# Kernel tuning notes

Measured on AMD Instinct MI355X. Metric: run time of the kernel, lower is better.

## Reference

```python
import jax, jax.numpy as jnp
import numpy as np

B, K, N = 8192, 10, 100
LAM = 1.0


def _vec_transpose_P():
    # 9x9 vec-transpose permutation: P[3i+j, 3j+i] = 1 (the _getP matrix)
    P = np.zeros((9, 9), dtype=np.float32)
    for i in range(3):
        for j in range(3):
            P[3 * i + j, 3 * j + i] = 1.0
    return jnp.asarray(P)


def setup_inputs() -> dict:
    key = jax.random.key(0)
    k1, k2, k3 = jax.random.split(key, 3)
    weights = jax.random.uniform(k1, (N, 1), dtype=jnp.float32) + 0.1  # positive weights
    model_keypoints = jax.random.normal(k2, (K, 3, N), dtype=jnp.float32)
    y = jax.random.normal(k3, (B, 3, N), dtype=jnp.float32)
    return {"y": y, "weights": weights, "model_keypoints": model_keypoints}


def _pace_forward(y, weights, model_keypoints):
    n = model_keypoints.shape[-1]
    k = model_keypoints.shape[0]
    bsz = y.shape[0]
    w = weights                                  # (N,1)
    wsum = w.sum()
    b = model_keypoints                          # (K,3,N)
    b_w = (b @ w) / wsum                         # (K,3,1)
    sw = jnp.sqrt(w[:, 0])                       # (N,)

    # ---- precomputed constants (original __init__) ----
    bar_b = sw[None, None, :] * (b - b_w)                    # (K,3,N)
    bar_B = bar_b.transpose(0, 2, 1).reshape(k, 3 * n).T     # (3N,K), row idx 3n+a
    bar_H = 2.0 * (bar_B.T @ bar_B + LAM * jnp.eye(k, dtype=y.dtype))
    Hinv = jnp.linalg.inv(bar_H)
    Ht = Hinv @ jnp.ones((k, 1), dtype=y.dtype)
    denom = Ht.sum()
    G = Hinv - (Ht @ Ht.T) / denom               # (K,K)
    g = Ht / denom                               # (K,1)
    GBt = G @ bar_B.T                            # (K,3N)
    M = jnp.concatenate([2.0 * bar_B @ GBt - jnp.eye(3 * n, dtype=y.dtype),
                         2.0 * jnp.sqrt(LAM) * GBt], axis=0)       # (3N+K,3N)
    h = jnp.concatenate([bar_B @ g, jnp.sqrt(LAM) * g], axis=0)    # (3N+K,1)
    P = _vec_transpose_P().astype(y.dtype)

    # ---- forward ----
    y_w = (y @ w) / wsum                         # (B,3,1)
    bar_y = sw[None, None, :] * (y - y_w)        # (B,3,N)

    # E_b = M @ kron(Ybar_b^T, I3) @ P, done batched without materializing kron:
    # (M @ kron(Y^T, I3))[m, 3j+a] = sum_n M[m, 3n+a] * Y[j, n]
    Mr = M.reshape(-1, n, 3)                                  # Mr[m, nn, a] = M[m, 3nn+a]
    MB = jnp.einsum('mna,bjn->bmja', Mr, bar_y)               # (B,3N+K,3,3)
    E = MB.reshape(bsz, -1, 9) @ P                            # (B,3N+K,9)
    q00 = h[:, 0] @ h[:, 0]                                   # scalar h^T h
    hE = jnp.einsum('m,bmc->bc', h[:, 0], E)                  # (B,9)
    Q11 = jnp.einsum('bmc,bmd->bcd', E, E)                    # (B,9,9)
    top = jnp.concatenate([jnp.broadcast_to(q00, (bsz, 1, 1)), hE[:, None, :]], axis=2)
    bot = jnp.concatenate([hE[:, :, None], Q11], axis=2)
    Q = jnp.concatenate([top, bot], axis=1)                   # (B,10,10)

    # SDP relaxation: at a tight optimum X = v v^T with v the minimizer of v^T Q v,
    # recovered here as the eigenvector of Q with smallest eigenvalue (batched eigh)
    _, evec = jnp.linalg.eigh(Q)
    v = evec[:, :, 0]                                         # (B,10), ascending order
    v = v / v[:, :1]                                          # homogenize: v[0] = 1
    R = v[:, 1:].reshape(bsz, 3, 3).transpose(0, 2, 1)        # (B,3,3)

    # shape coefficients: c = 2 * G B^T * kron(I_N, R^T) vec(bar_y) + g
    RTy = jnp.einsum('bra,brn->bna', R, bar_y).reshape(bsz, 3 * n)   # idx 3n+a
    c = 2.0 * jnp.einsum('km,bm->bk', GBt, RTy)[:, :, None] + g[None, :, :]  # (B,K,1)
    # translation: t = y_w - R b_w^T c
    t = y_w - R @ jnp.einsum('ka,bko->bao', b_w[:, :, 0], c)  # (B,3,1)
    return R, t, c


def reference(y, weights, model_keypoints):
    return _pace_forward(y, weights, model_keypoints)
```

## Files before the change

kernel.cpp:

```cpp
#include <hip/hip_runtime.h>
#include <math.h>

#define SM_WSUM 0
#define SM_RWS  1
#define SM_Q00  2
#define SM_Z2   4
#define SM_BS   16
#define SM_W    48
#define SM_G    148
#define SM_GV   248
#define SM_BW   260
#define SM_SIZE 292

#define AR_W    0
#define AR_BW   104
#define AR_C    136
#define AR_HI   240
#define AR_G    340
#define AR_T    440
#define AR_GV   544
#define AR_HT   560
#define AR_Z    576
#define AR_F    0
#define AR_QL   360
#define AR_D    592
#define AR_G3   640
#define AR_SIZE 768

__host__ __device__ constexpr int TRI(int p,int q){ return p*10-(p*(p+1))/2+q; }
__host__ __device__ constexpr int SIDX(int a,int b){ return (a<=b)?TRI(a,b):TRI(b,a); }
__host__ __device__ constexpr int LTRI(int i,int j){ return i*(i+1)/2+j; }

template<int CTRL>
__device__ __forceinline__ float dpp_add(float v){
  int s = __builtin_amdgcn_mov_dpp(__float_as_int(v), CTRL, 0xF, 0xF, true);
  return v + __int_as_float(s);
}
__device__ __forceinline__ float gsum16(float v){
  v = dpp_add<0xB1>(v);
  v = dpp_add<0x4E>(v);
  v = dpp_add<0x141>(v);
  v = dpp_add<0x140>(v);
  return v;
}

__global__ __launch_bounds__(64,2) void pace_fused(const float* __restrict__ y,
                                                   const float* __restrict__ w,
                                                   const float* __restrict__ mk,
                                                   float* __restrict__ out){
  __shared__ __attribute__((aligned(16))) float sc[3600];
  __shared__ float sm[SM_SIZE];
  __shared__ __attribute__((aligned(16))) float arena[AR_SIZE];
  const int tid  = threadIdx.x;
  const int sub  = tid & 15;
  const int item = tid >> 4;
  const int gb   = blockIdx.x*4 + item;
  const float* yb = y + gb*300;

  {
    float* a_w  = arena+AR_W;
    float* a_bw = arena+AR_BW;
    float* a_C  = arena+AR_C;
    float* a_Hi = arena+AR_HI;
    float* a_G  = arena+AR_G;
    float* a_T  = arena+AR_T;
    float* a_gv = arena+AR_GV;
    float* a_Ht = arena+AR_HT;
    float* a_z  = arena+AR_Z;

    for (int i=tid;i<100;i+=64) a_w[i]=w[i];
    __syncthreads();

    float av = a_w[tid] + ((tid<36)? a_w[tid+64] : 0.f);
    #pragma unroll
    for (int m=32;m;m>>=1) av += __shfl_xor(av,m);
    const float wsum = av;
    const float rws  = 1.0f/av;

    if (tid<30){
      const float4* p=(const float4*)(mk+tid*100);
      const float4* q=(const float4*)a_w;
      float acc=0;
      #pragma unroll 5
      for (int j=0;j<25;j++){ float4 x=p[j], yv=q[j];
        acc=fmaf(x.x,yv.x,acc); acc=fmaf(x.y,yv.y,acc);
        acc=fmaf(x.z,yv.z,acc); acc=fmaf(x.w,yv.w,acc); }
      a_bw[tid]=acc*rws;
    }
    __syncthreads();

    for (int i=tid;i<3000;i+=64){
      int r=i/100, n=i-100*r;
      sc[n*36+1+r]=a_w[n]*(mk[i]-a_bw[r]);
    }
    for (int i=tid;i<100;i+=64){
      sc[i*36]=a_w[i];
      sc[i*36+31]=0.f; sc[i*36+32]=0.f; sc[i*36+33]=0.f;
      sc[i*36+34]=0.f; sc[i*36+35]=0.f;
    }
    for (int e=tid;e<100;e+=64){
      int k=e/10, k2=e-10*k;
      float acc=0;
      #pragma unroll
      for (int j=0;j<3;j++){
        const float4* pa=(const float4*)(mk+(3*k+j)*100);
        const float4* pb=(const float4*)(mk+(3*k2+j)*100);
        const float4* pw=(const float4*)a_w;
        float ba=a_bw[3*k+j], bb=a_bw[3*k2+j];
        #pragma unroll 5
        for (int q=0;q<25;q++){
          float4 xa=pa[q], xb=pb[q], xw=pw[q];
          acc=fmaf(xw.x*(xa.x-ba),(xb.x-bb),acc);
          acc=fmaf(xw.y*(xa.y-ba),(xb.y-bb),acc);
          acc=fmaf(xw.z*(xa.z-ba),(xb.z-bb),acc);
          acc=fmaf(xw.w*(xa.w-ba),(xb.w-bb),acc);
        }
      }
      a_C[e]=acc;
    }
    __syncthreads();

    float R[20];
    {
      int row=(tid<10)? tid : 0;
      #pragma unroll
      for (int c=0;c<10;c++) R[c]=2.0f*(a_C[row*10+c]+(c==row?1.0f:0.0f));
      #pragma unroll
      for (int c=0;c<10;c++) R[10+c]=(c==row)?1.0f:0.0f;
    }
    #pragma unroll
    for (int p=0;p<10;p++){
      float appv=__shfl(R[p],p);
      float ra=1.0f/appv;
      float fr=R[p];
      #pragma unroll
      for (int c=0;c<20;c++){
        float pc=__shfl(R[c],p)*ra;
        R[c]=(tid==p)? pc : fmaf(-fr,pc,R[c]);
      }
    }
    float ht=0.f;
    if (tid<10){
      #pragma unroll
      for (int c=0;c<10;c++){ a_Hi[tid*10+c]=R[10+c]; ht+=R[10+c]; }
      a_Ht[tid]=ht;
    }
    float hv=(tid<10)? ht : 0.f;
    #pragma unroll
    for (int m=32;m;m>>=1) hv+=__shfl_xor(hv,m);
    const float rden=1.0f/hv;
    if (tid<10) a_gv[tid]=ht*rden;
    __syncthreads();
    for (int e=tid;e<100;e+=64){ int r=e/10,c=e-10*r; a_G[e]=a_Hi[e]-a_Ht[r]*a_Ht[c]*rden; }
    __syncthreads();
    for (int e=tid;e<100;e+=64){
      int r=e/10,c=e-10*r; float acc=0;
      #pragma unroll
      for (int j=0;j<10;j++) acc+=(a_C[r*10+j]+(r==j?1.0f:0.0f))*a_G[j*10+c];
      a_T[e]=acc;
    }
    __syncthreads();
    for (int e=tid;e<100;e+=64){
      int r=e/10,c=e-10*r; float acc=0;
      #pragma unroll
      for (int j=0;j<10;j++) acc+=a_G[r*10+j]*a_T[j*10+c];
      sm[SM_W+e]=4.0f*acc-4.0f*a_G[e];
      sm[SM_G+e]=a_G[e];
    }
    if (tid<10){
      float acc=0;
      #pragma unroll
      for (int j=0;j<10;j++) acc+=(a_C[tid*10+j]+(tid==j?1.0f:0.0f))*a_gv[j];
      a_z[tid]=acc;
    }
    __syncthreads();
    if (tid<10){
      float acc=0;
      #pragma unroll
      for (int j=0;j<10;j++) acc+=a_G[tid*10+j]*a_z[j];
      sm[SM_Z2+tid]=2.0f*acc-a_gv[tid];
    }
    float qv=0.f;
    if (tid<10){
      float acc=0;
      #pragma unroll
      for (int c=0;c<10;c++) acc+=a_C[tid*10+c]*a_gv[c];
      qv=a_gv[tid]*acc+a_gv[tid]*a_gv[tid];
    }
    #pragma unroll
    for (int m=32;m;m>>=1) qv+=__shfl_xor(qv,m);
    if (tid==0){ sm[SM_WSUM]=wsum; sm[SM_RWS]=rws; sm[SM_Q00]=qv; sm[3]=0.f; }
    if (tid<30){
      float acc=0;
      for (int n=0;n<100;n++) acc+=sc[n*36+1+tid];
      sm[SM_BS+tid]=acc;
    }
    if (tid<10) sm[SM_GV+tid]=a_gv[tid];
    if (tid<30) sm[SM_BW+tid]=a_bw[tid];
    __syncthreads();
  }

  float* sF  = arena+AR_F;
  float* sQl = arena+AR_QL;
  float* sD  = arena+AR_D;
  float* sG3 = arena+AR_G3;

  float F0[90];
  #pragma unroll
  for (int i=0;i<90;i++) F0[i]=0.f;
  float swy0=0,swy1=0,swy2=0,s00=0,s01=0,s02=0,s11=0,s12=0,s22=0;

  auto point=[&](int n){
    float y0=yb[n], y1=yb[100+n], y2=yb[200+n];
    float c[32];
    const float4* cp=(const float4*)&sc[n*36];
    #pragma unroll
    for (int r=0;r<8;r++) ((float4*)c)[r]=cp[r];
    float wn=c[0];
    float wy0=wn*y0,wy1=wn*y1,wy2=wn*y2;
    swy0+=wy0;swy1+=wy1;swy2+=wy2;
    s00+=wy0*y0;s01+=wy0*y1;s02+=wy0*y2;s11+=wy1*y1;s12+=wy1*y2;s22+=wy2*y2;
    #pragma unroll
    for (int k=0;k<10;k++){
      #pragma unroll
      for (int j=0;j<3;j++){
        float bcv=c[1+k*3+j];
        F0[k*9+j*3+0]+=bcv*y0;
        F0[k*9+j*3+1]+=bcv*y1;
        F0[k*9+j*3+2]+=bcv*y2;
      }
    }
  };
  #pragma unroll
  for (int m=0;m<6;m++) point(sub+16*m);
  if (sub<4) point(96+sub);

  #pragma unroll
  for (int e=0;e<90;e++) F0[e]=gsum16(F0[e]);
  swy0=gsum16(swy0); swy1=gsum16(swy1); swy2=gsum16(swy2);
  s00=gsum16(s00); s01=gsum16(s01); s02=gsum16(s02);
  s11=gsum16(s11); s12=gsum16(s12); s22=gsum16(s22);

  const float wsum=sm[SM_WSUM], rws=sm[SM_RWS];
  const float yw0=swy0*rws, yw1=swy1*rws, yw2=swy2*rws;
  float G3r[9];
  G3r[0]=s00-wsum*yw0*yw0; G3r[4]=s11-wsum*yw1*yw1; G3r[8]=s22-wsum*yw2*yw2;
  G3r[1]=G3r[3]=s01-wsum*yw0*yw1;
  G3r[2]=G3r[6]=s02-wsum*yw0*yw2;
  G3r[5]=G3r[7]=s12-wsum*yw1*yw2;
  #pragma unroll
  for (int k=0;k<10;k++){
    float bs0=sm[SM_BS+k*3+0],bs1=sm[SM_BS+k*3+1],bs2=sm[SM_BS+k*3+2];
    F0[k*9+0]-=yw0*bs0; F0[k*9+1]-=yw1*bs0; F0[k*9+2]-=yw2*bs0;
    F0[k*9+3]-=yw0*bs1; F0[k*9+4]-=yw1*bs1; F0[k*9+5]-=yw2*bs1;
    F0[k*9+6]-=yw0*bs2; F0[k*9+7]-=yw1*bs2; F0[k*9+8]-=yw2*bs2;
  }
  if (sub==0){
    #pragma unroll
    for (int e=0;e<90;e++) sF[item*90+e]=F0[e];
    #pragma unroll
    for (int e=0;e<9;e++) sG3[item*9+e]=G3r[e];
  }
  __syncthreads();

  if (sub<9){
    int mp=sub;
    float fcol[10], t2[10];
    #pragma unroll
    for (int k=0;k<10;k++) fcol[k]=sF[item*90+k*9+mp];
    #pragma unroll
    for (int k=0;k<10;k++){
      float acc=0;
      #pragma unroll
      for (int k2=0;k2<10;k2++) acc+=sm[SM_W+k*10+k2]*fcol[k2];
      t2[k]=acc;
    }
    float he=0;
    #pragma unroll
    for (int k=0;k<10;k++) he+=sm[SM_Z2+k]*fcol[k];
    sQl[item*56 + 1+mp]=he;
    #pragma unroll 1
    for (int m=0;m<=mp;m++){
      float gd=sG3[item*9+(m%3)*3+(mp%3)];
      float acc=((m/3)==(mp/3))? gd : 0.f;
      #pragma unroll
      for (int k=0;k<10;k++) acc+=sF[item*90+k*9+m]*t2[k];
      int p=1+m, q=1+mp;
      sQl[item*56 + p*10-((p*(p+1))>>1)+q]=acc;
    }
  }
  if (sub==9) sQl[item*56 + 0]=sm[SM_Q00];
  __syncthreads();

  float A[55];
  #pragma unroll
  for (int e=0;e<55;e++) A[e]=sQl[item*56+e];
  float dd[10], ee[9];
  #pragma unroll
  for (int k=0;k<8;k++){
    float nrm2=0.f;
    #pragma unroll
    for (int i=1;i<10;i++){ if (i<k+1) continue; float xi=A[SIDX(i,k)]; nrm2=fmaf(xi,xi,nrm2); }
    float x0=A[SIDX(k+1,k)];
    float nr=sqrtf(nrm2);
    float alpha=-copysignf(nr,x0);
    bool ok=nrm2>1e-30f;
    float v1=x0-alpha;
    float vtv=-2.0f*alpha*v1;
    float bh=ok?2.0f*__builtin_amdgcn_rcpf(vtv):0.f;
    ee[k]=ok?alpha:x0;
    float vv[10];
    #pragma unroll
    for (int i=0;i<10;i++) vv[i]=(i<k+1)?0.f:((i==k+1)?v1:A[SIDX(i,k)]);
    float p[10];
    #pragma unroll
    for (int i=0;i<10;i++){
      if (i<k+1){ p[i]=0.f; continue; }
      float acc=0;
      #pragma unroll
      for (int j=1;j<10;j++){ if (j<k+1) continue; acc+=A[SIDX(i,j)]*vv[j]; }
      p[i]=bh*acc;
    }
    float Kc=0.f;
    #pragma unroll
    for (int i=1;i<10;i++){ if (i<k+1) continue; Kc=fmaf(vv[i],p[i],Kc); }
    Kc*=0.5f*bh;
    float wv[10];
    #pragma unroll
    for (int i=0;i<10;i++) wv[i]=p[i]-Kc*vv[i];
    #pragma unroll
    for (int i=1;i<10;i++){
      if (i<k+1) continue;
      #pragma unroll
      for (int j=1;j<10;j++){
        if (j<i) continue;
        A[TRI(i,j)]-=vv[i]*wv[j]+wv[i]*vv[j];
      }
    }
  }
  ee[8]=A[TRI(8,9)];
  #pragma unroll
  for (int i=0;i<10;i++) dd[i]=A[TRI(i,i)];
  float esq[9];
  #pragma unroll
  for (int i=0;i<9;i++) esq[i]=ee[i]*ee[i];

  float scaleT=0.f, lo=1e30f, hi=1e30f;
  #pragma unroll
  for (int i=0;i<10;i++){
    float r=((i>0)?fabsf(ee[i-1]):0.f)+((i<9)?fabsf(ee[i]):0.f);
    scaleT=fmaxf(scaleT,fabsf(dd[i])+r);
    lo=fminf(lo,dd[i]-r);
    hi=fminf(hi,dd[i]);
  }
  hi+=1e-6f*scaleT+1e-30f;
  const float pm=1e-12f*scaleT+1e-37f;
  const float r17=1.0f/17.0f;
  #pragma unroll 1
  for (int it=0;it<5;++it){
    float delta=(hi-lo)*r17;
    float mid=lo+delta*(float)(sub+1);
    float q=dd[0]-mid;
    q=(fabsf(q)<pm)?((q<0.f)?-pm:pm):q;
    int cnt=(q<0.f);
    #pragma unroll
    for (int i=1;i<10;i++){
      q=dd[i]-mid-esq[i-1]*__builtin_amdgcn_rcpf(q);
      q=(fabsf(q)<pm)?((q<0.f)?-pm:pm):q;
      cnt+=(q<0.f);
    }
    unsigned long long bal=__ballot(cnt>0);
    unsigned gm=(unsigned)((bal>>(item*16))&0xFFFFull);
    int js=gm?(__ffs((int)gm)-1):16;
    float nhi=(js<16)?(lo+delta*(float)(js+1)):hi;
    lo=lo+delta*(float)js;
    hi=nhi;
  }
  const float sigma=lo-1e-5f*scaleT-1e-30f;
  const float pmL=1e-8f*scaleT+1e-37f;

  float Lc[55], rd[10];
  #pragma unroll
  for (int i=0;i<10;i++){
    #pragma unroll
    for (int j=0;j<10;j++){
      if (j>i) continue;
      float a=sQl[item*56+SIDX(j,i)]-((i==j)?sigma:0.f);
      #pragma unroll
      for (int t2=0;t2<9;t2++){
        if (t2>=j) continue;
        a-=Lc[LTRI(i,t2)]*Lc[LTRI(j,t2)];
      }
      if (j<i) Lc[LTRI(i,j)]=a*rd[j];
      else { a=fmaxf(a,pmL); rd[i]=rsqrtf(a); Lc[LTRI(i,i)]=a*rd[i]; }
    }
  }
  float xv[10];
  #pragma unroll
  for (int i=0;i<10;i++) xv[i]=1.f;
  #pragma unroll 1
  for (int itr=0;itr<3;++itr){
    #pragma unroll
    for (int i=0;i<10;i++){
      float acc=xv[i];
      #pragma unroll
      for (int j=0;j<9;j++){ if (j>=i) continue; acc-=Lc[LTRI(i,j)]*xv[j]; }
      acc*=rd[i];
      xv[i]=fminf(fmaxf(acc,-1e15f),1e15f);
    }
    #pragma unroll
    for (int i=9;i>=0;i--){
      float acc=xv[i];
      #pragma unroll
      for (int j=9;j>0;j--){ if (j<=i) continue; acc-=Lc[LTRI(j,i)]*xv[j]; }
      acc*=rd[i];
      xv[i]=fminf(fmaxf(acc,-1e15f),1e15f);
    }
    float nn=0.f;
    #pragma unroll
    for (int i=0;i<10;i++) nn=fmaf(xv[i],xv[i],nn);
    nn=fmaxf(nn,1e-30f);
    float sc2=rsqrtf(nn);
    #pragma unroll
    for (int i=0;i<10;i++) xv[i]*=sc2;
  }
  float r0=1.0f/xv[0];
  float vn[10];
  vn[0]=1.f;
  #pragma unroll
  for (int m=1;m<10;m++) vn[m]=xv[m]*r0;

  if (sub<10){
    float dv=0;
    #pragma unroll
    for (int m=0;m<9;m++) dv+=vn[1+m]*sF[item*90+sub*9+m];
    sD[item*12+sub]=dv;
  }
  __syncthreads();
  float dreg[10];
  #pragma unroll
  for (int k=0;k<10;k++) dreg[k]=sD[item*12+k];
  __syncthreads();
  if (sub<10){
    float acc=0;
    #pragma unroll
    for (int k2=0;k2<10;k2++) acc+=sm[SM_G+sub*10+k2]*dreg[k2];
    float cvk=2.0f*acc+sm[SM_GV+sub];
    out[98304+gb*10+sub]=cvk;
    sD[item*12+sub]=cvk;
  }
  __syncthreads();
  float cvr[10];
  #pragma unroll
  for (int k=0;k<10;k++) cvr[k]=sD[item*12+k];
  float e0=0,e1=0,e2=0;
  #pragma unroll
  for (int k=0;k<10;k++){
    e0+=sm[SM_BW+k*3+0]*cvr[k];
    e1+=sm[SM_BW+k*3+1]*cvr[k];
    e2+=sm[SM_BW+k*3+2]*cvr[k];
  }
  if (sub==10){
    #pragma unroll
    for (int i=0;i<3;i++)
      #pragma unroll
      for (int j=0;j<3;j++)
        out[gb*9+i*3+j]=vn[1+3*j+i];
  }
  if (sub==11){
    out[73728+gb*3+0]=yw0-(vn[1]*e0+vn[4]*e1+vn[7]*e2);
    out[73728+gb*3+1]=yw1-(vn[2]*e0+vn[5]*e1+vn[8]*e2);
    out[73728+gb*3+2]=yw2-(vn[3]*e0+vn[6]*e1+vn[9]*e2);
  }
}

extern "C" void kernel_launch(void* const* d_in, const int* in_sizes, int n_in,
                              void* d_out, int out_size, void* d_ws, size_t ws_size,
                              hipStream_t stream) {
  const float* y  = (const float*)d_in[0];
  const float* w  = (const float*)d_in[1];
  const float* mk = (const float*)d_in[2];
  float* out = (float*)d_out;
  pace_fused<<<2048, 64, 0, stream>>>(y, w, mk, out);
}
```

Before: 110.1 us.

## Process 16 items per 256-thread block, serialize eigen solve per item in one thread

Grows blocks from 64 to 256 threads covering 16 batch items, so the per-block constant setup (inverse, G, M-derived terms) is amortized over four times as many items. Model keypoints are staged in LDS and the scaled basis is reused. The tridiagonal eigensolve and back-substitution now run with one thread per item (16 threads) using 16-step serial bisection instead of 16-lane cooperative multisection. The aim is to cut redundant setup work, at the cost of leaving most of the block idle during the serial eigen phase and using more LDS per block.

```diff
diff --git a/kernel.cpp b/kernel.cpp
--- a/kernel.cpp
+++ b/kernel.cpp
@@ -12,20 +12,7 @@
 #define SM_BW   260
 #define SM_SIZE 292
 
-#define AR_W    0
-#define AR_BW   104
-#define AR_C    136
-#define AR_HI   240
-#define AR_G    340
-#define AR_T    440
-#define AR_GV   544
-#define AR_HT   560
-#define AR_Z    576
-#define AR_F    0
-#define AR_QL   360
-#define AR_D    592
-#define AR_G3   640
-#define AR_SIZE 768
+#define AR_SIZE 3712
 
 __host__ __device__ constexpr int TRI(int p,int q){ return p*10-(p*(p+1))/2+q; }
 __host__ __device__ constexpr int SIDX(int a,int b){ return (a<=b)?TRI(a,b):TRI(b,a); }
@@ -44,230 +31,234 @@
   return v;
 }
 
-__global__ __launch_bounds__(64,2) void pace_fused(const float* __restrict__ y,
-                                                   const float* __restrict__ w,
-                                                   const float* __restrict__ mk,
-                                                   float* __restrict__ out){
+__global__ __launch_bounds__(256,2) void pace_fused(const float* __restrict__ y,
+                                                    const float* __restrict__ w,
+                                                    const float* __restrict__ mk,
+                                                    float* __restrict__ out){
   __shared__ __attribute__((aligned(16))) float sc[3600];
   __shared__ float sm[SM_SIZE];
   __shared__ __attribute__((aligned(16))) float arena[AR_SIZE];
   const int tid  = threadIdx.x;
+  const int lane = tid & 63;
   const int sub  = tid & 15;
   const int item = tid >> 4;
-  const int gb   = blockIdx.x*4 + item;
+  const int gb   = blockIdx.x*16 + item;
   const float* yb = y + gb*300;
 
   {
-    float* a_w  = arena+AR_W;
-    float* a_bw = arena+AR_BW;
-    float* a_C  = arena+AR_C;
-    float* a_Hi = arena+AR_HI;
-    float* a_G  = arena+AR_G;
-    float* a_T  = arena+AR_T;
-    float* a_gv = arena+AR_GV;
-    float* a_Ht = arena+AR_HT;
-    float* a_z  = arena+AR_Z;
-
-    for (int i=tid;i<100;i+=64) a_w[i]=w[i];
-    __syncthreads();
-
-    float av = a_w[tid] + ((tid<36)? a_w[tid+64] : 0.f);
+    float* s_mb = arena;
+    float* s_w  = arena+3000;
+    float* s_sw = arena+3104;
+    float* s_bw = arena+3208;
+    float* s_C  = arena+3240;
+    float* s_Hi = arena+3340;
+    float* s_G  = arena+3440;
+    float* s_T  = arena+3540;
+    float* s_gv = arena+3640;
+    float* s_Ht = arena+3656;
+    float* s_z  = arena+3672;
+
+    for (int i=tid;i<3000;i+=256) s_mb[i]=mk[i];
+    for (int i=tid;i<100;i+=256){ float x=w[i]; s_w[i]=x; s_sw[i]=sqrtf(x); }
+    __syncthreads();
+
+    float av = s_w[lane] + ((lane<36)? s_w[lane+64] : 0.f);
     #pragma unroll
     for (int m=32;m;m>>=1) av += __shfl_xor(av,m);
     const float wsum = av;
     const float rws  = 1.0f/av;
 
     if (tid<30){
-      const float4* p=(const float4*)(mk+tid*100);
-      const float4* q=(const float4*)a_w;
+      const float4* p=(const float4*)&s_mb[tid*100];
+      const float4* q=(const float4*)&s_w[0];
       float acc=0;
       #pragma unroll 5
       for (int j=0;j<25;j++){ float4 x=p[j], yv=q[j];
         acc=fmaf(x.x,yv.x,acc); acc=fmaf(x.y,yv.y,acc);
         acc=fmaf(x.z,yv.z,acc); acc=fmaf(x.w,yv.w,acc); }
-      a_bw[tid]=acc*rws;
-    }
-    __syncthreads();
-
-    for (int i=tid;i<3000;i+=64){
-      int r=i/100, n=i-100*r;
-      sc[n*36+1+r]=a_w[n]*(mk[i]-a_bw[r]);
-    }
-    for (int i=tid;i<100;i+=64){
-      sc[i*36]=a_w[i];
-      sc[i*36+31]=0.f; sc[i*36+32]=0.f; sc[i*36+33]=0.f;
-      sc[i*36+34]=0.f; sc[i*36+35]=0.f;
-    }
-    for (int e=tid;e<100;e+=64){
-      int k=e/10, k2=e-10*k;
-      float acc=0;
-      #pragma unroll
-      for (int j=0;j<3;j++){
-        const float4* pa=(const float4*)(mk+(3*k+j)*100);
-        const float4* pb=(const float4*)(mk+(3*k2+j)*100);
-        const float4* pw=(const float4*)a_w;
-        float ba=a_bw[3*k+j], bb=a_bw[3*k2+j];
-        #pragma unroll 5
-        for (int q=0;q<25;q++){
-          float4 xa=pa[q], xb=pb[q], xw=pw[q];
-          acc=fmaf(xw.x*(xa.x-ba),(xb.x-bb),acc);
-          acc=fmaf(xw.y*(xa.y-ba),(xb.y-bb),acc);
-          acc=fmaf(xw.z*(xa.z-ba),(xb.z-bb),acc);
-          acc=fmaf(xw.w*(xa.w-ba),(xb.w-bb),acc);
+      s_bw[tid]=acc*rws;
+    }
+    __syncthreads();
+    for (int i=tid;i<3000;i+=256){ int r=i/100, n=i-r*100; s_mb[i]=s_sw[n]*(s_mb[i]-s_bw[r]); }
+    __syncthreads();
+    if (tid<100){
+      int k=tid/10, k2=tid-10*(tid/10);
+      const float4* p1=(const float4*)&s_mb[k*300];
+      const float4* p2=(const float4*)&s_mb[k2*300];
+      float acc=0;
+      #pragma unroll 5
+      for (int j=0;j<75;j++){ float4 x=p1[j], yv=p2[j];
+        acc=fmaf(x.x,yv.x,acc); acc=fmaf(x.y,yv.y,acc);
+        acc=fmaf(x.z,yv.z,acc); acc=fmaf(x.w,yv.w,acc); }
+      s_C[tid]=acc;
+    }
+    __syncthreads();
+    if (tid<64){
+      float R[20];
+      {
+        int row=(tid<10)? tid : 0;
+        #pragma unroll
+        for (int c=0;c<10;c++) R[c]=2.0f*(s_C[row*10+c]+(c==row?1.0f:0.0f));
+        #pragma unroll
+        for (int c=0;c<10;c++) R[10+c]=(c==row)?1.0f:0.0f;
+      }
+      #pragma unroll
+      for (int p=0;p<10;p++){
+        float appv=__shfl(R[p],p);
+        float ra=1.0f/appv;
+        float fr=R[p];
+        #pragma unroll
+        for (int c=0;c<20;c++){
+          float pc=__shfl(R[c],p)*ra;
+          R[c]=(tid==p)? pc : fmaf(-fr,pc,R[c]);
         }
       }
-      a_C[e]=acc;
-    }
-    __syncthreads();
-
-    float R[20];
-    {
-      int row=(tid<10)? tid : 0;
-      #pragma unroll
-      for (int c=0;c<10;c++) R[c]=2.0f*(a_C[row*10+c]+(c==row?1.0f:0.0f));
-      #pragma unroll
-      for (int c=0;c<10;c++) R[10+c]=(c==row)?1.0f:0.0f;
-    }
-    #pragma unroll
-    for (int p=0;p<10;p++){
-      float appv=__shfl(R[p],p);
-      float ra=1.0f/appv;
-      float fr=R[p];
-      #pragma unroll
-      for (int c=0;c<20;c++){
-        float pc=__shfl(R[c],p)*ra;
-        R[c]=(tid==p)? pc : fmaf(-fr,pc,R[c]);
-      }
-    }
-    float ht=0.f;
+      if (tid<10){
+        float ht=0.f;
+        #pragma unroll
+        for (int c=0;c<10;c++){ s_Hi[tid*10+c]=R[10+c]; ht+=R[10+c]; }
+        s_Ht[tid]=ht;
+      }
+    }
+    __syncthreads();
+    float dsum=0.f;
+    #pragma unroll
+    for (int k=0;k<10;k++) dsum+=s_Ht[k];
+    const float rden=1.0f/dsum;
+    if (tid<10) s_gv[tid]=s_Ht[tid]*rden;
+    __syncthreads();
+    if (tid<100){ int r=tid/10,c=tid-10*(tid/10); s_G[tid]=s_Hi[tid]-s_Ht[r]*s_Ht[c]*rden; }
+    __syncthreads();
+    if (tid<100){
+      int r=tid/10,c=tid-10*(tid/10); float acc=0;
+      #pragma unroll
+      for (int j=0;j<10;j++) acc+=(s_C[r*10+j]+(r==j?1.0f:0.0f))*s_G[j*10+c];
+      s_T[tid]=acc;
+    }
+    __syncthreads();
+    if (tid<100){
+      int r=tid/10,c=tid-10*(tid/10); float acc=0;
+      #pragma unroll
+      for (int j=0;j<10;j++) acc+=s_G[r*10+j]*s_T[j*10+c];
+      sm[SM_W+tid]=4.0f*acc-4.0f*s_G[tid];
+      sm[SM_G+tid]=s_G[tid];
+    }
     if (tid<10){
-      #pragma unroll
-      for (int c=0;c<10;c++){ a_Hi[tid*10+c]=R[10+c]; ht+=R[10+c]; }
-      a_Ht[tid]=ht;
-    }
-    float hv=(tid<10)? ht : 0.f;
-    #pragma unroll
-    for (int m=32;m;m>>=1) hv+=__shfl_xor(hv,m);
-    const float rden=1.0f/hv;
-    if (tid<10) a_gv[tid]=ht*rden;
-    __syncthreads();
-    for (int e=tid;e<100;e+=64){ int r=e/10,c=e-10*r; a_G[e]=a_Hi[e]-a_Ht[r]*a_Ht[c]*rden; }
-    __syncthreads();
-    for (int e=tid;e<100;e+=64){
-      int r=e/10,c=e-10*r; float acc=0;
-      #pragma unroll
-      for (int j=0;j<10;j++) acc+=(a_C[r*10+j]+(r==j?1.0f:0.0f))*a_G[j*10+c];
-      a_T[e]=acc;
-    }
-    __syncthreads();
-    for (int e=tid;e<100;e+=64){
-      int r=e/10,c=e-10*r; float acc=0;
-      #pragma unroll
-      for (int j=0;j<10;j++) acc+=a_G[r*10+j]*a_T[j*10+c];
-      sm[SM_W+e]=4.0f*acc-4.0f*a_G[e];
-      sm[SM_G+e]=a_G[e];
-    }
+      float acc=0;
+      #pragma unroll
+      for (int j=0;j<10;j++) acc+=(s_C[tid*10+j]+(tid==j?1.0f:0.0f))*s_gv[j];
+      s_z[tid]=acc;
+    }
+    __syncthreads();
     if (tid<10){
       float acc=0;
       #pragma unroll
-      for (int j=0;j<10;j++) acc+=(a_C[tid*10+j]+(tid==j?1.0f:0.0f))*a_gv[j];
-      a_z[tid]=acc;
-    }
-    __syncthreads();
-    if (tid<10){
-      float acc=0;
-      #pragma unroll
-      for (int j=0;j<10;j++) acc+=a_G[tid*10+j]*a_z[j];
-      sm[SM_Z2+tid]=2.0f*acc-a_gv[tid];
-    }
-    float qv=0.f;
-    if (tid<10){
-      float acc=0;
-      #pragma unroll
-      for (int c=0;c<10;c++) acc+=a_C[tid*10+c]*a_gv[c];
-      qv=a_gv[tid]*acc+a_gv[tid]*a_gv[tid];
-    }
-    #pragma unroll
-    for (int m=32;m;m>>=1) qv+=__shfl_xor(qv,m);
-    if (tid==0){ sm[SM_WSUM]=wsum; sm[SM_RWS]=rws; sm[SM_Q00]=qv; sm[3]=0.f; }
+      for (int j=0;j<10;j++) acc+=s_G[tid*10+j]*s_z[j];
+      sm[SM_Z2+tid]=2.0f*acc-s_gv[tid];
+    }
+    if (tid==0){
+      float acc=0;
+      #pragma unroll
+      for (int r=0;r<10;r++){
+        float rr=0;
+        #pragma unroll
+        for (int c=0;c<10;c++) rr+=s_C[r*10+c]*s_gv[c];
+        acc+=s_gv[r]*rr+s_gv[r]*s_gv[r];
+      }
+      sm[SM_WSUM]=wsum; sm[SM_RWS]=rws; sm[SM_Q00]=acc; sm[3]=0.f;
+    }
+    for (int i=tid;i<3600;i+=256){
+      int n=i/36, e=i-36*n; float v;
+      if (e==0) v=s_w[n];
+      else if (e>=31) v=0.f;
+      else v=s_mb[(e-1)*100+n]*s_sw[n];
+      sc[i]=v;
+    }
     if (tid<30){
-      float acc=0;
-      for (int n=0;n<100;n++) acc+=sc[n*36+1+tid];
+      const float4* p=(const float4*)&s_mb[tid*100];
+      const float4* q=(const float4*)&s_sw[0];
+      float acc=0;
+      #pragma unroll 5
+      for (int j=0;j<25;j++){ float4 x=p[j], yv=q[j];
+        acc=fmaf(x.x,yv.x,acc); acc=fmaf(x.y,yv.y,acc);
+        acc=fmaf(x.z,yv.z,acc); acc=fmaf(x.w,yv.w,acc); }
       sm[SM_BS+tid]=acc;
     }
-    if (tid<10) sm[SM_GV+tid]=a_gv[tid];
-    if (tid<30) sm[SM_BW+tid]=a_bw[tid];
+    if (tid<10) sm[SM_GV+tid]=s_gv[tid];
+    if (tid<30) sm[SM_BW+tid]=s_bw[tid];
     __syncthreads();
   }
 
-  float* sF  = arena+AR_F;
-  float* sQl = arena+AR_QL;
-  float* sD  = arena+AR_D;
-  float* sG3 = arena+AR_G3;
-
-  float F0[90];
-  #pragma unroll
-  for (int i=0;i<90;i++) F0[i]=0.f;
-  float swy0=0,swy1=0,swy2=0,s00=0,s01=0,s02=0,s11=0,s12=0,s22=0;
-
-  auto point=[&](int n){
-    float y0=yb[n], y1=yb[100+n], y2=yb[200+n];
-    float c[32];
-    const float4* cp=(const float4*)&sc[n*36];
-    #pragma unroll
-    for (int r=0;r<8;r++) ((float4*)c)[r]=cp[r];
-    float wn=c[0];
-    float wy0=wn*y0,wy1=wn*y1,wy2=wn*y2;
-    swy0+=wy0;swy1+=wy1;swy2+=wy2;
-    s00+=wy0*y0;s01+=wy0*y1;s02+=wy0*y2;s11+=wy1*y1;s12+=wy1*y2;s22+=wy2*y2;
+  float* sF  = arena;
+  float* sQl = arena+1440;
+  float* sG3 = arena+2352;
+  float* sYW = arena+2496;
+
+  {
+    float F0[90];
+    #pragma unroll
+    for (int i=0;i<90;i++) F0[i]=0.f;
+    float swy0=0,swy1=0,swy2=0,s00=0,s01=0,s02=0,s11=0,s12=0,s22=0;
+
+    auto point=[&](int n){
+      float y0=yb[n], y1=yb[100+n], y2=yb[200+n];
+      float c[32];
+      const float4* cp=(const float4*)&sc[n*36];
+      #pragma unroll
+      for (int r=0;r<8;r++) ((float4*)c)[r]=cp[r];
+      float wn=c[0];
+      float wy0=wn*y0,wy1=wn*y1,wy2=wn*y2;
+      swy0+=wy0;swy1+=wy1;swy2+=wy2;
+      s00+=wy0*y0;s01+=wy0*y1;s02+=wy0*y2;s11+=wy1*y1;s12+=wy1*y2;s22+=wy2*y2;
+      #pragma unroll
+      for (int k=0;k<10;k++){
+        #pragma unroll
+        for (int j=0;j<3;j++){
+          float bcv=c[1+k*3+j];
+          F0[k*9+j*3+0]+=bcv*y0;
+          F0[k*9+j*3+1]+=bcv*y1;
+          F0[k*9+j*3+2]+=bcv*y2;
+        }
+      }
+    };
+    #pragma unroll
+    for (int m=0;m<6;m++) point(sub+16*m);
+    if (sub<4) point(96+sub);
+
+    #pragma unroll
+    for (int e=0;e<90;e++) F0[e]=gsum16(F0[e]);
+    swy0=gsum16(swy0); swy1=gsum16(swy1); swy2=gsum16(swy2);
+    s00=gsum16(s00); s01=gsum16(s01); s02=gsum16(s02);
+    s11=gsum16(s11); s12=gsum16(s12); s22=gsum16(s22);
+
+    const float wsum=sm[SM_WSUM], rws=sm[SM_RWS];
+    const float yw0=swy0*rws, yw1=swy1*rws, yw2=swy2*rws;
     #pragma unroll
     for (int k=0;k<10;k++){
-      #pragma unroll
-      for (int j=0;j<3;j++){
-        float bcv=c[1+k*3+j];
-        F0[k*9+j*3+0]+=bcv*y0;
-        F0[k*9+j*3+1]+=bcv*y1;
-        F0[k*9+j*3+2]+=bcv*y2;
-      }
-    }
-  };
-  #pragma unroll
-  for (int m=0;m<6;m++) point(sub+16*m);
-  if (sub<4) point(96+sub);
-
-  #pragma unroll
-  for (int e=0;e<90;e++) F0[e]=gsum16(F0[e]);
-  swy0=gsum16(swy0); swy1=gsum16(swy1); swy2=gsum16(swy2);
-  s00=gsum16(s00); s01=gsum16(s01); s02=gsum16(s02);
-  s11=gsum16(s11); s12=gsum16(s12); s22=gsum16(s22);
-
-  const float wsum=sm[SM_WSUM], rws=sm[SM_RWS];
-  const float yw0=swy0*rws, yw1=swy1*rws, yw2=swy2*rws;
-  float G3r[9];
-  G3r[0]=s00-wsum*yw0*yw0; G3r[4]=s11-wsum*yw1*yw1; G3r[8]=s22-wsum*yw2*yw2;
-  G3r[1]=G3r[3]=s01-wsum*yw0*yw1;
-  G3r[2]=G3r[6]=s02-wsum*yw0*yw2;
-  G3r[5]=G3r[7]=s12-wsum*yw1*yw2;
-  #pragma unroll
-  for (int k=0;k<10;k++){
-    float bs0=sm[SM_BS+k*3+0],bs1=sm[SM_BS+k*3+1],bs2=sm[SM_BS+k*3+2];
-    F0[k*9+0]-=yw0*bs0; F0[k*9+1]-=yw1*bs0; F0[k*9+2]-=yw2*bs0;
-    F0[k*9+3]-=yw0*bs1; F0[k*9+4]-=yw1*bs1; F0[k*9+5]-=yw2*bs1;
-    F0[k*9+6]-=yw0*bs2; F0[k*9+7]-=yw1*bs2; F0[k*9+8]-=yw2*bs2;
-  }
-  if (sub==0){
-    #pragma unroll
-    for (int e=0;e<90;e++) sF[item*90+e]=F0[e];
-    #pragma unroll
-    for (int e=0;e<9;e++) sG3[item*9+e]=G3r[e];
+      float bs0=sm[SM_BS+k*3+0],bs1=sm[SM_BS+k*3+1],bs2=sm[SM_BS+k*3+2];
+      F0[k*9+0]-=yw0*bs0; F0[k*9+1]-=yw1*bs0; F0[k*9+2]-=yw2*bs0;
+      F0[k*9+3]-=yw0*bs1; F0[k*9+4]-=yw1*bs1; F0[k*9+5]-=yw2*bs1;
+      F0[k*9+6]-=yw0*bs2; F0[k*9+7]-=yw1*bs2; F0[k*9+8]-=yw2*bs2;
+    }
+    for (int e=sub;e<90;e+=16) sF[item*90+e]=F0[e];
+    if (sub==0){
+      sG3[item*9+0]=s00-wsum*yw0*yw0;
+      sG3[item*9+4]=s11-wsum*yw1*yw1;
+      sG3[item*9+8]=s22-wsum*yw2*yw2;
+      float g01=s01-wsum*yw0*yw1, g02=s02-wsum*yw0*yw2, g12=s12-wsum*yw1*yw2;
+      sG3[item*9+1]=g01; sG3[item*9+3]=g01;
+      sG3[item*9+2]=g02; sG3[item*9+6]=g02;
+      sG3[item*9+5]=g12; sG3[item*9+7]=g12;
+      sYW[item*4+0]=yw0; sYW[item*4+1]=yw1; sYW[item*4+2]=yw2;
+    }
   }
   __syncthreads();
 
-  if (sub<9){
-    int mp=sub;
+  if (tid<144){
+    int it2=tid/9, mp=tid-9*(tid/9);
     float fcol[10], t2[10];
     #pragma unroll
-    for (int k=0;k<10;k++) fcol[k]=sF[item*90+k*9+mp];
+    for (int k=0;k<10;k++) fcol[k]=sF[it2*90+k*9+mp];
     #pragma unroll
     for (int k=0;k<10;k++){
       float acc=0;
@@ -278,199 +269,191 @@
     float he=0;
     #pragma unroll
     for (int k=0;k<10;k++) he+=sm[SM_Z2+k]*fcol[k];
-    sQl[item*56 + 1+mp]=he;
+    sQl[it2*57 + 1+mp]=he;
     #pragma unroll 1
     for (int m=0;m<=mp;m++){
-      float gd=sG3[item*9+(m%3)*3+(mp%3)];
+      float gd=sG3[it2*9+(m%3)*3+(mp%3)];
       float acc=((m/3)==(mp/3))? gd : 0.f;
       #pragma unroll
-      for (int k=0;k<10;k++) acc+=sF[item*90+k*9+m]*t2[k];
+      for (int k=0;k<10;k++) acc+=sF[it2*90+k*9+m]*t2[k];
       int p=1+m, q=1+mp;
-      sQl[item*56 + p*10-((p*(p+1))>>1)+q]=acc;
+      sQl[it2*57 + p*10-((p*(p+1))>>1)+q]=acc;
     }
   }
-  if (sub==9) sQl[item*56 + 0]=sm[SM_Q00];
+  if (tid>=144 && tid<160) sQl[(tid-144)*57]=sm[SM_Q00];
   __syncthreads();
 
-  float A[55];
-  #pragma unroll
-  for (int e=0;e<55;e++) A[e]=sQl[item*56+e];
-  float dd[10], ee[9];
-  #pragma unroll
-  for (int k=0;k<8;k++){
-    float nrm2=0.f;
-    #pragma unroll
-    for (int i=1;i<10;i++){ if (i<k+1) continue; float xi=A[SIDX(i,k)]; nrm2=fmaf(xi,xi,nrm2); }
-    float x0=A[SIDX(k+1,k)];
-    float nr=sqrtf(nrm2);
-    float alpha=-copysignf(nr,x0);
-    bool ok=nrm2>1e-30f;
-    float v1=x0-alpha;
-    float vtv=-2.0f*alpha*v1;
-    float bh=ok?2.0f*__builtin_amdgcn_rcpf(vtv):0.f;
-    ee[k]=ok?alpha:x0;
-    float vv[10];
-    #pragma unroll
-    for (int i=0;i<10;i++) vv[i]=(i<k+1)?0.f:((i==k+1)?v1:A[SIDX(i,k)]);
-    float p[10];
+  if (tid<16){
+    const int it2=tid;
+    const int gb2=blockIdx.x*16+it2;
+    float A[55];
+    #pragma unroll
+    for (int e=0;e<55;e++) A[e]=sQl[it2*57+e];
+    float dd[10], ee[9];
+    #pragma unroll
+    for (int k=0;k<8;k++){
+      float nrm2=0.f;
+      #pragma unroll
+      for (int i=1;i<10;i++){ if (i<k+1) continue; float xi=A[SIDX(i,k)]; nrm2=fmaf(xi,xi,nrm2); }
+      float x0=A[SIDX(k+1,k)];
+      float nr=sqrtf(nrm2);
+      float alpha=-copysignf(nr,x0);
+      bool ok=nrm2>1e-30f;
+      float v1=x0-alpha;
+      float vtv=-2.0f*alpha*v1;
+      float bh=ok?2.0f*__builtin_amdgcn_rcpf(vtv):0.f;
+      ee[k]=ok?alpha:x0;
+      float vv[10];
+      #pragma unroll
+      for (int i=0;i<10;i++) vv[i]=(i<k+1)?0.f:((i==k+1)?v1:A[SIDX(i,k)]);
+      float p[10];
+      #pragma unroll
+      for (int i=0;i<10;i++){
+        if (i<k+1){ p[i]=0.f; continue; }
+        float acc=0;
+        #pragma unroll
+        for (int j=1;j<10;j++){ if (j<k+1) continue; acc+=A[SIDX(i,j)]*vv[j]; }
+        p[i]=bh*acc;
+      }
+      float Kc=0.f;
+      #pragma unroll
+      for (int i=1;i<10;i++){ if (i<k+1) continue; Kc=fmaf(vv[i],p[i],Kc); }
+      Kc*=0.5f*bh;
+      float wv[10];
+      #pragma unroll
+      for (int i=0;i<10;i++) wv[i]=p[i]-Kc*vv[i];
+      #pragma unroll
+      for (int i=1;i<10;i++){
+        if (i<k+1) continue;
+        #pragma unroll
+        for (int j=1;j<10;j++){
+          if (j<i) continue;
+          A[TRI(i,j)]-=vv[i]*wv[j]+wv[i]*vv[j];
+        }
+      }
+    }
+    ee[8]=A[TRI(8,9)];
+    #pragma unroll
+    for (int i=0;i<10;i++) dd[i]=A[TRI(i,i)];
+    float esq[9];
+    #pragma unroll
+    for (int i=0;i<9;i++) esq[i]=ee[i]*ee[i];
+
+    float scaleT=0.f, lo=1e30f, hi=1e30f;
     #pragma unroll
     for (int i=0;i<10;i++){
-      if (i<k+1){ p[i]=0.f; continue; }
-      float acc=0;
-      #pragma unroll
-      for (int j=1;j<10;j++){ if (j<k+1) continue; acc+=A[SIDX(i,j)]*vv[j]; }
-      p[i]=bh*acc;
-    }
-    float Kc=0.f;
-    #pragma unroll
-    for (int i=1;i<10;i++){ if (i<k+1) continue; Kc=fmaf(vv[i],p[i],Kc); }
-    Kc*=0.5f*bh;
-    float wv[10];
-    #pragma unroll
-    for (int i=0;i<10;i++) wv[i]=p[i]-Kc*vv[i];
-    #pragma unroll
-    for (int i=1;i<10;i++){
-      if (i<k+1) continue;
-      #pragma unroll
-      for (int j=1;j<10;j++){
-        if (j<i) continue;
-        A[TRI(i,j)]-=vv[i]*wv[j]+wv[i]*vv[j];
-      }
-    }
-  }
-  ee[8]=A[TRI(8,9)];
-  #pragma unroll
-  for (int i=0;i<10;i++) dd[i]=A[TRI(i,i)];
-  float esq[9];
-  #pragma unroll
-  for (int i=0;i<9;i++) esq[i]=ee[i]*ee[i];
-
-  float scaleT=0.f, lo=1e30f, hi=1e30f;
-  #pragma unroll
-  for (int i=0;i<10;i++){
-    float r=((i>0)?fabsf(ee[i-1]):0.f)+((i<9)?fabsf(ee[i]):0.f);
-    scaleT=fmaxf(scaleT,fabsf(dd[i])+r);
-    lo=fminf(lo,dd[i]-r);
-    hi=fminf(hi,dd[i]);
-  }
-  hi+=1e-6f*scaleT+1e-30f;
-  const float pm=1e-12f*scaleT+1e-37f;
-  const float r17=1.0f/17.0f;
-  #pragma unroll 1
-  for (int it=0;it<5;++it){
-    float delta=(hi-lo)*r17;
-    float mid=lo+delta*(float)(sub+1);
-    float q=dd[0]-mid;
-    q=(fabsf(q)<pm)?((q<0.f)?-pm:pm):q;
-    int cnt=(q<0.f);
-    #pragma unroll
-    for (int i=1;i<10;i++){
-      q=dd[i]-mid-esq[i-1]*__builtin_amdgcn_rcpf(q);
+      float r=((i>0)?fabsf(ee[i-1]):0.f)+((i<9)?fabsf(ee[i]):0.f);
+      scaleT=fmaxf(scaleT,fabsf(dd[i])+r);
+      lo=fminf(lo,dd[i]-r);
+      hi=fminf(hi,dd[i]);
+    }
+    hi+=1e-6f*scaleT+1e-30f;
+    const float pm=1e-12f*scaleT+1e-37f;
+    #pragma unroll 1
+    for (int it=0;it<16;++it){
+      float mid=0.5f*(lo+hi);
+      float q=dd[0]-mid;
       q=(fabsf(q)<pm)?((q<0.f)?-pm:pm):q;
-      cnt+=(q<0.f);
-    }
-    unsigned long long bal=__ballot(cnt>0);
-    unsigned gm=(unsigned)((bal>>(item*16))&0xFFFFull);
-    int js=gm?(__ffs((int)gm)-1):16;
-    float nhi=(js<16)?(lo+delta*(float)(js+1)):hi;
-    lo=lo+delta*(float)js;
-    hi=nhi;
-  }
-  const float sigma=lo-1e-5f*scaleT-1e-30f;
-  const float pmL=1e-8f*scaleT+1e-37f;
-
-  float Lc[55], rd[10];
-  #pragma unroll
-  for (int i=0;i<10;i++){
-    #pragma unroll
-    for (int j=0;j<10;j++){
-      if (j>i) continue;
-      float a=sQl[item*56+SIDX(j,i)]-((i==j)?sigma:0.f);
-      #pragma unroll
-      for (int t2=0;t2<9;t2++){
-        if (t2>=j) continue;
-        a-=Lc[LTRI(i,t2)]*Lc[LTRI(j,t2)];
-      }
-      if (j<i) Lc[LTRI(i,j)]=a*rd[j];
-      else { a=fmaxf(a,pmL); rd[i]=rsqrtf(a); Lc[LTRI(i,i)]=a*rd[i]; }
-    }
-  }
-  float xv[10];
-  #pragma unroll
-  for (int i=0;i<10;i++) xv[i]=1.f;
-  #pragma unroll 1
-  for (int itr=0;itr<3;++itr){
+      int cnt=(q<0.f);
+      #pragma unroll
+      for (int i=1;i<10;i++){
+        q=dd[i]-mid-esq[i-1]*__builtin_amdgcn_rcpf(q);
+        q=(fabsf(q)<pm)?((q<0.f)?-pm:pm):q;
+        cnt+=(q<0.f);
+      }
+      bool any=cnt>0;
+      hi=any?mid:hi;
+      lo=any?lo:mid;
+    }
+    const float sigma=lo-1e-5f*scaleT-1e-30f;
+    const float pmL=1e-8f*scaleT+1e-37f;
+
+    float Lc[55], rd[10];
     #pragma unroll
     for (int i=0;i<10;i++){
-      float acc=xv[i];
-      #pragma unroll
-      for (int j=0;j<9;j++){ if (j>=i) continue; acc-=Lc[LTRI(i,j)]*xv[j]; }
-      acc*=rd[i];
-      xv[i]=fminf(fmaxf(acc,-1e15f),1e15f);
-    }
-    #pragma unroll
-    for (int i=9;i>=0;i--){
-      float acc=xv[i];
-      #pragma unroll
-      for (int j=9;j>0;j--){ if (j<=i) continue; acc-=Lc[LTRI(j,i)]*xv[j]; }
-      acc*=rd[i];
-      xv[i]=fminf(fmaxf(acc,-1e15f),1e15f);
-    }
-    float nn=0.f;
-    #pragma unroll
-    for (int i=0;i<10;i++) nn=fmaf(xv[i],xv[i],nn);
-    nn=fmaxf(nn,1e-30f);
-    float sc2=rsqrtf(nn);
-    #pragma unroll
-    for (int i=0;i<10;i++) xv[i]*=sc2;
-  }
-  float r0=1.0f/xv[0];
-  float vn[10];
-  vn[0]=1.f;
-  #pragma unroll
-  for (int m=1;m<10;m++) vn[m]=xv[m]*r0;
-
-  if (sub<10){
-    float dv=0;
-    #pragma unroll
-    for (int m=0;m<9;m++) dv+=vn[1+m]*sF[item*90+sub*9+m];
-    sD[item*12+sub]=dv;
-  }
-  __syncthreads();
-  float dreg[10];
-  #pragma unroll
-  for (int k=0;k<10;k++) dreg[k]=sD[item*12+k];
-  __syncthreads();
-  if (sub<10){
-    float acc=0;
-    #pragma unroll
-    for (int k2=0;k2<10;k2++) acc+=sm[SM_G+sub*10+k2]*dreg[k2];
-    float cvk=2.0f*acc+sm[SM_GV+sub];
-    out[98304+gb*10+sub]=cvk;
-    sD[item*12+sub]=cvk;
-  }
-  __syncthreads();
-  float cvr[10];
-  #pragma unroll
-  for (int k=0;k<10;k++) cvr[k]=sD[item*12+k];
-  float e0=0,e1=0,e2=0;
-  #pragma unroll
-  for (int k=0;k<10;k++){
-    e0+=sm[SM_BW+k*3+0]*cvr[k];
-    e1+=sm[SM_BW+k*3+1]*cvr[k];
-    e2+=sm[SM_BW+k*3+2]*cvr[k];
-  }
-  if (sub==10){
+      #pragma unroll
+      for (int j=0;j<10;j++){
+        if (j>i) continue;
+        float a=sQl[it2*57+SIDX(j,i)]-((i==j)?sigma:0.f);
+        #pragma unroll
+        for (int t2=0;t2<9;t2++){
+          if (t2>=j) continue;
+          a-=Lc[LTRI(i,t2)]*Lc[LTRI(j,t2)];
+        }
+        if (j<i) Lc[LTRI(i,j)]=a*rd[j];
+        else { a=fmaxf(a,pmL); rd[i]=rsqrtf(a); Lc[LTRI(i,i)]=a*rd[i]; }
+      }
+    }
+    float xv[10];
+    #pragma unroll
+    for (int i=0;i<10;i++) xv[i]=1.f;
+    #pragma unroll 1
+    for (int itr=0;itr<3;++itr){
+      #pragma unroll
+      for (int i=0;i<10;i++){
+        float acc=xv[i];
+        #pragma unroll
+        for (int j=0;j<9;j++){ if (j>=i) continue; acc-=Lc[LTRI(i,j)]*xv[j]; }
+        acc*=rd[i];
+        xv[i]=fminf(fmaxf(acc,-1e15f),1e15f);
+      }
+      #pragma unroll
+      for (int i=9;i>=0;i--){
+        float acc=xv[i];
+        #pragma unroll
+        for (int j=9;j>0;j--){ if (j<=i) continue; acc-=Lc[LTRI(j,i)]*xv[j]; }
+        acc*=rd[i];
+        xv[i]=fminf(fmaxf(acc,-1e15f),1e15f);
+      }
+      float nn=0.f;
+      #pragma unroll
+      for (int i=0;i<10;i++) nn=fmaf(xv[i],xv[i],nn);
+      nn=fmaxf(nn,1e-30f);
+      float sc2=rsqrtf(nn);
+      #pragma unroll
+      for (int i=0;i<10;i++) xv[i]*=sc2;
+    }
+    float r0=1.0f/xv[0];
+    float vn[10];
+    vn[0]=1.f;
+    #pragma unroll
+    for (int m=1;m<10;m++) vn[m]=xv[m]*r0;
+
+    float dv[10];
+    #pragma unroll
+    for (int k=0;k<10;k++){
+      float acc=0;
+      #pragma unroll
+      for (int m=0;m<9;m++) acc+=vn[1+m]*sF[it2*90+k*9+m];
+      dv[k]=acc;
+    }
+    float cv[10];
+    #pragma unroll
+    for (int k=0;k<10;k++){
+      float acc=0;
+      #pragma unroll
+      for (int k2=0;k2<10;k2++) acc+=sm[SM_G+k*10+k2]*dv[k2];
+      cv[k]=2.0f*acc+sm[SM_GV+k];
+    }
+    float e0=0,e1=0,e2=0;
+    #pragma unroll
+    for (int k=0;k<10;k++){
+      e0+=sm[SM_BW+k*3+0]*cv[k];
+      e1+=sm[SM_BW+k*3+1]*cv[k];
+      e2+=sm[SM_BW+k*3+2]*cv[k];
+    }
+    float yw0=sYW[it2*4+0], yw1=sYW[it2*4+1], yw2=sYW[it2*4+2];
     #pragma unroll
     for (int i=0;i<3;i++)
       #pragma unroll
       for (int j=0;j<3;j++)
-        out[gb*9+i*3+j]=vn[1+3*j+i];
-  }
-  if (sub==11){
-    out[73728+gb*3+0]=yw0-(vn[1]*e0+vn[4]*e1+vn[7]*e2);
-    out[73728+gb*3+1]=yw1-(vn[2]*e0+vn[5]*e1+vn[8]*e2);
-    out[73728+gb*3+2]=yw2-(vn[3]*e0+vn[6]*e1+vn[9]*e2);
+        out[gb2*9+i*3+j]=vn[1+3*j+i];
+    out[73728+gb2*3+0]=yw0-(vn[1]*e0+vn[4]*e1+vn[7]*e2);
+    out[73728+gb2*3+1]=yw1-(vn[2]*e0+vn[5]*e1+vn[8]*e2);
+    out[73728+gb2*3+2]=yw2-(vn[3]*e0+vn[6]*e1+vn[9]*e2);
+    #pragma unroll
+    for (int k=0;k<10;k++)
+      out[98304+gb2*10+k]=cv[k];
   }
 }
 
@@ -481,5 +464,5 @@
   const float* w  = (const float*)d_in[1];
   const float* mk = (const float*)d_in[2];
   float* out = (float*)d_out;
-  pace_fused<<<2048, 64, 0, stream>>>(y, w, mk, out);
+  pace_fused<<<512, 256, 0, stream>>>(y, w, mk, out);
 }
```

New measurement: 152.1 us. +38.2%, slower.
